# Optimization experiments

Measured on AMD Instinct MI355X. Metric: run time of the kernel, lower is better.

The kernel has to match this reference:

```python
import jax, jax.numpy as jnp
import numpy as np

GAM1 = 1.0
GAM2 = 1.0
EPS = 0.01


def setup_inputs() -> dict:
    key = jax.random.key(0)
    k1, k2 = jax.random.split(key)
    m, p, k = 262144, 128, 10
    x = jax.random.normal(k1, (m, p), dtype=jnp.float32)
    y = jax.random.randint(k2, (m,), 0, k, dtype=jnp.int32)
    return {"x": x, "y": y, "num_classes": k}


def reference(x, y, num_classes):
    m, p = x.shape
    I = jnp.eye(p, dtype=x.dtype)
    scalar = p / (m * EPS)

    # W = x.T, so W @ W.T == x.T @ x  (p x p Gram)
    cov = x.T @ x
    discrimn_empi = jnp.linalg.slogdet(I + GAM1 * scalar * cov)[1] / 2.0
    discrimn_theo = jnp.linalg.slogdet(I + scalar * cov)[1] / 2.0

    # per-class compress loss: logdet(I + p/(n_j*eps) * W_j W_j^T) * n_j / m
    onehot = jax.nn.one_hot(y, num_classes, dtype=x.dtype)  # [m, k]
    counts = onehot.sum(axis=0)                             # [k]

    def class_cov(col):  # col: [m] 0/1 mask for one class
        return (x * col[:, None]).T @ x  # [p, p]

    covs = jax.lax.map(class_cov, onehot.T)  # [k, p, p], sequential over k classes

    safe_counts = jnp.maximum(counts, 1.0)
    scal = p / (safe_counts * EPS)                              # [k]
    lds = jnp.linalg.slogdet(I[None] + scal[:, None, None] * covs)[1]  # [k]
    compress = jnp.sum(jnp.where(counts > 0, lds * counts / m, 0.0)) / 2.0

    total_loss_empi = GAM2 * (-discrimn_empi) + compress
    return total_loss_empi, discrimn_empi, discrimn_theo, compress
```

## Files before the change

### kernel.cpp

```cpp
#include <hip/hip_runtime.h>

#define K 10
#define P 128
#define EPSV 0.01f
#define GAM1 1.0f
#define GAM2 1.0f
#define CH 256
#define SK 32
#define KS 36
#define NSTG (CH / SK)
#define SORTCH 2048
#define NTHR 256

typedef __attribute__((ext_vector_type(8))) short bf16x8;
typedef __attribute__((ext_vector_type(4))) short s16x4;
typedef __attribute__((ext_vector_type(4))) float f32x4;

static __device__ __forceinline__ short f2bf(float f) {
    unsigned u = __float_as_uint(f);
    u = (u + 0x7FFFu + ((u >> 16) & 1u)) >> 16;
    return (short)u;
}

static __device__ __forceinline__ float rdlane(float v, int srclane) {
    return __int_as_float(__builtin_amdgcn_readlane(__float_as_int(v), srclane));
}

__global__ void hist_kernel(const int* __restrict__ y, int* __restrict__ blk_counts, int m) {
    __shared__ int h[K];
    int t = threadIdx.x;
    if (t < K) h[t] = 0;
    __syncthreads();
    int base = blockIdx.x * SORTCH;
    int rows = min(SORTCH, m - base);
    for (int i = t; i < rows; i += NTHR) atomicAdd(&h[y[base + i]], 1);
    __syncthreads();
    if (t < K) blk_counts[blockIdx.x * K + t] = h[t];
}

__global__ void scan_kernel(const int* __restrict__ blk_counts, int* __restrict__ blk_offsets,
                            int* __restrict__ counts, int* __restrict__ pstart, int nb) {
    __shared__ int s[K][128];
    __shared__ int sps[K + 1];
    int t = threadIdx.x;
    int own[K];
    if (t < 128) {
        for (int c = 0; c < K; ++c) {
            int v = (t < nb) ? blk_counts[t * K + c] : 0;
            own[c] = v;
            s[c][t] = v;
        }
    }
    __syncthreads();
    for (int off = 1; off < 128; off <<= 1) {
        int tmp[K];
        if (t < 128)
            for (int c = 0; c < K; ++c) tmp[c] = (t >= off) ? s[c][t - off] : 0;
        __syncthreads();
        if (t < 128)
            for (int c = 0; c < K; ++c) s[c][t] += tmp[c];
        __syncthreads();
    }
    if (t == 0) {
        int run = 0;
        for (int c = 0; c < K; ++c) {
            sps[c] = run;
            int tot = s[c][127];
            counts[c] = tot;
            pstart[c] = run;
            run += ((tot + CH - 1) / CH) * CH;
        }
        sps[K] = run;
        pstart[K] = run;
    }
    __syncthreads();
    if (t < nb)
        for (int c = 0; c < K; ++c)
            blk_offsets[t * K + c] = sps[c] + s[c][t] - own[c];
}

__global__ void scatter_kernel(const int* __restrict__ y, const int* __restrict__ blk_offsets,
                               int* __restrict__ perm, int m) {
    __shared__ int cur[K];
    int t = threadIdx.x;
    if (t < K) cur[t] = blk_offsets[blockIdx.x * K + t];
    __syncthreads();
    int base = blockIdx.x * SORTCH;
    int rows = min(SORTCH, m - base);
    for (int i = t; i < rows; i += NTHR) {
        int row = base + i;
        int pos = atomicAdd(&cur[y[row]], 1);
        perm[pos] = row;
    }
}

__global__ __launch_bounds__(NTHR, 4) void gram_kernel(const float* __restrict__ x,
                                                       const int* __restrict__ perm,
                                                       const int* __restrict__ pstart,
                                                       const int* __restrict__ counts,
                                                       float* __restrict__ grams) {
    __shared__ int pm[CH];
    __shared__ short xsT[2][P * KS];
    int t = threadIdx.x;
    int base = blockIdx.x * CH;
    int cls = 0;
#pragma unroll
    for (int c = 1; c < K; ++c)
        if (base >= pstart[c]) cls = c;
    const int limit = pstart[cls] + counts[cls];
    pm[t] = perm[base + t];

    const int lane = t & 63;
    const int wave = t >> 6;
    const int m16 = lane & 15;
    const int quad = lane >> 4;
    const int wr = wave >> 1;
    const int wc = wave & 1;
    const int c2 = lane;

    f32x4 acc[4][4];
#pragma unroll
    for (int a = 0; a < 4; ++a)
#pragma unroll
        for (int b = 0; b < 4; ++b) acc[a][b] = (f32x4){0.f, 0.f, 0.f, 0.f};

    __syncthreads();

    float2 v[8];
#pragma unroll
    for (int ii = 0; ii < 8; ++ii) {
        int pos = wave * 8 + ii;
        float2 val; val.x = 0.f; val.y = 0.f;
        if (base + pos < limit) {
            int r = pm[pos];
            val = ((const float2*)(x + (size_t)r * P))[c2];
        }
        v[ii] = val;
    }

#pragma unroll 2
    for (int s = 0; s < NSTG; ++s) {
        short* xb = &xsT[s & 1][0];
        short b0[8], b1[8];
#pragma unroll
        for (int ii = 0; ii < 8; ++ii) { b0[ii] = f2bf(v[ii].x); b1[ii] = f2bf(v[ii].y); }
        {
            int col0 = 2 * c2, col1 = 2 * c2 + 1;
            int kb = wave * 8;
#pragma unroll
            for (int q = 0; q < 2; ++q) {
                s16x4 w0 = {b0[q * 4], b0[q * 4 + 1], b0[q * 4 + 2], b0[q * 4 + 3]};
                s16x4 w1 = {b1[q * 4], b1[q * 4 + 1], b1[q * 4 + 2], b1[q * 4 + 3]};
                *(s16x4*)&xb[col0 * KS + kb + q * 4] = w0;
                *(s16x4*)&xb[col1 * KS + kb + q * 4] = w1;
            }
        }
        __syncthreads();
        if (s + 1 < NSTG) {
            int sb = (s + 1) * SK;
#pragma unroll
            for (int ii = 0; ii < 8; ++ii) {
                int pos = sb + wave * 8 + ii;
                float2 val; val.x = 0.f; val.y = 0.f;
                if (base + pos < limit) {
                    int r = pm[pos];
                    val = ((const float2*)(x + (size_t)r * P))[c2];
                }
                v[ii] = val;
            }
        }
        int k0 = quad * 8;
        bf16x8 bfr[4];
#pragma unroll
        for (int b = 0; b < 4; ++b) {
            int colB = wc * 64 + b * 16 + m16;
            union { bf16x8 v8; s16x4 h[2]; } u;
            u.h[0] = *(const s16x4*)&xb[colB * KS + k0];
            u.h[1] = *(const s16x4*)&xb[colB * KS + k0 + 4];
            bfr[b] = u.v8;
        }
#pragma unroll
        for (int a = 0; a < 4; ++a) {
            int colA = wr * 64 + a * 16 + m16;
            union { bf16x8 v8; s16x4 h[2]; } u;
            u.h[0] = *(const s16x4*)&xb[colA * KS + k0];
            u.h[1] = *(const s16x4*)&xb[colA * KS + k0 + 4];
            bf16x8 af = u.v8;
#pragma unroll
            for (int b = 0; b < 4; ++b)
                acc[a][b] = __builtin_amdgcn_mfma_f32_16x16x32_bf16(af, bfr[b], acc[a][b], 0, 0, 0);
        }
    }
    float* g = grams + (size_t)cls * P * P;
#pragma unroll
    for (int a = 0; a < 4; ++a)
#pragma unroll
        for (int b = 0; b < 4; ++b)
#pragma unroll
            for (int r = 0; r < 4; ++r) {
                int gi = wr * 64 + a * 16 + quad * 4 + r;
                int gj = wc * 64 + b * 16 + m16;
                if (gi <= gj) atomicAdd(&g[gi * P + gj], acc[a][b][r]);
            }
}

__global__ void sum_kernel(const float* __restrict__ grams, float* __restrict__ gsum) {
    int idx = blockIdx.x * 256 + threadIdx.x;
    float s = 0.f;
#pragma unroll
    for (int c = 0; c < K; ++c) s += grams[c * P * P + idx];
    gsum[idx] = s;
}

__global__ __launch_bounds__(256, 1) void logdet_kernel(const float* __restrict__ grams,
                                                        const float* __restrict__ gsum,
                                                        const int* __restrict__ counts,
                                                        float* __restrict__ logd, int m) {
    __shared__ float A[P * P];
    int t = threadIdx.x, b = blockIdx.x;
    float scale;
    if (b == 0) scale = GAM1 * (float)P / ((float)m * EPSV);
    else if (b == 1) scale = (float)P / ((float)m * EPSV);
    else {
        float cnt = (float)counts[b - 2];
        if (cnt < 1.f) cnt = 1.f;
        scale = (float)P / (cnt * EPSV);
    }
    const float* src = (b < 2) ? gsum : (grams + (size_t)(b - 2) * P * P);
    for (int idx = t; idx < P * P; idx += 256) {
        int i = idx >> 7, c = idx & (P - 1);
        int s2 = (i <= c) ? idx : (c * P + i);
        A[idx] = scale * src[s2] + ((i == c) ? 1.f : 0.f);
    }
    __syncthreads();

    const int lane = t & 63;
    const int wid = t >> 6;
    float lsum = 0.f;

    for (int bs = 0; bs < 4; ++bs) {
        const int j0 = bs * 32;
        if (wid == 0) {
            float a[32];
            if (lane < 32) {
#pragma unroll
                for (int cc = 0; cc < 8; ++cc)
                    *(f32x4*)&a[cc * 4] = *(f32x4*)&A[(j0 + lane) * P + j0 + cc * 4];
            } else {
#pragma unroll
                for (int cc = 0; cc < 32; ++cc) a[cc] = 0.f;
            }
            float myinv = 0.f;
#pragma unroll
            for (int tt = 0; tt < 32; ++tt) {
                float utt = rdlane(a[tt], tt);
                float inv = __builtin_amdgcn_rcpf(utt);
                lsum += __logf(utt);
                if (lane == tt) myinv = inv;
                bool act = (lane < 32) && (lane > tt);
                float lm = act ? a[tt] * inv : 0.f;
                if (act) a[tt] = lm;
#pragma unroll
                for (int k2 = tt + 1; k2 < 32; ++k2) {
                    float utk = rdlane(a[k2], tt);
                    a[k2] -= lm * utk;
                }
            }
            if (lane < 32) A[(j0 + lane) * P + j0 + lane] = myinv;

            if (bs < 3) {
                int nc = P - j0 - 32;
                int c0 = j0 + 32 + lane;
                int c1 = c0 + 64;
                bool v0 = lane < nc;
                bool v1 = lane + 64 < nc;
                int c0a = v0 ? c0 : (j0 + 32);
                int c1a = v1 ? c1 : (j0 + 32);
                float ua[32], ub[32];
#pragma unroll
                for (int j = 0; j < 32; ++j) {
                    ua[j] = A[(j0 + j) * P + c0a];
                    ub[j] = A[(j0 + j) * P + c1a];
                }
#pragma unroll
                for (int j = 0; j < 32; ++j) {
#pragma unroll
                    for (int t2 = 0; t2 < j; ++t2) {
                        float ljt = rdlane(a[t2], j);
                        ua[j] -= ljt * ua[t2];
                        ub[j] -= ljt * ub[t2];
                    }
                }
#pragma unroll
                for (int j = 0; j < 32; ++j) {
                    if (v0) A[(j0 + j) * P + c0] = ua[j];
                    if (v1) A[(j0 + j) * P + c1] = ub[j];
                }
            }
        }
        __syncthreads();

        if (bs < 3) {
            int nc = P - j0 - 32;
            int nt = nc >> 2;
            int ntiles = nt * nt;
            for (int tile = t; tile < ntiles; tile += 256) {
                int ti = tile / nt, tk = tile - ti * nt;
                int i0 = j0 + 32 + ti * 4, k0 = j0 + 32 + tk * 4;
                f32x4 acc0 = {0, 0, 0, 0}, acc1 = {0, 0, 0, 0};
                f32x4 acc2 = {0, 0, 0, 0}, acc3 = {0, 0, 0, 0};
#pragma unroll
                for (int j = 0; j < 32; ++j) {
                    const float* row = &A[(j0 + j) * P];
                    float invd = row[j0 + j];
                    f32x4 ui = *(const f32x4*)&row[i0];
                    f32x4 uk = *(const f32x4*)&row[k0];
                    uk *= invd;
                    acc0 += ui[0] * uk;
                    acc1 += ui[1] * uk;
                    acc2 += ui[2] * uk;
                    acc3 += ui[3] * uk;
                }
                f32x4* r0 = (f32x4*)&A[(i0 + 0) * P + k0];
                f32x4* r1 = (f32x4*)&A[(i0 + 1) * P + k0];
                f32x4* r2 = (f32x4*)&A[(i0 + 2) * P + k0];
                f32x4* r3 = (f32x4*)&A[(i0 + 3) * P + k0];
                *r0 -= acc0; *r1 -= acc1; *r2 -= acc2; *r3 -= acc3;
            }
            __syncthreads();
        }
    }
    if (t == 0) logd[b] = lsum;
}

__global__ void final_kernel(const float* __restrict__ logd, const int* __restrict__ counts,
                             float* __restrict__ out, int m) {
    if (threadIdx.x == 0 && blockIdx.x == 0) {
        float empi = 0.5f * logd[0];
        float theo = 0.5f * logd[1];
        float comp = 0.f;
        for (int c = 0; c < K; ++c) {
            float cnt = (float)counts[c];
            if (cnt > 0.f) comp += logd[2 + c] * cnt / (float)m;
        }
        comp *= 0.5f;
        out[0] = GAM2 * (-empi) + comp;
        out[1] = empi;
        out[2] = theo;
        out[3] = comp;
    }
}

extern "C" void kernel_launch(void* const* d_in, const int* in_sizes, int n_in,
                              void* d_out, int out_size, void* d_ws, size_t ws_size,
                              hipStream_t stream) {
    const float* x = (const float*)d_in[0];
    const int* y = (const int*)d_in[1];
    int m = in_sizes[1];
    int nbs = (m + SORTCH - 1) / SORTCH;
    int nbg = (m + CH - 1) / CH + K;

    char* ws = (char*)d_ws;
    float* grams = (float*)ws;
    float* gsum = (float*)(ws + 655360);
    float* logd = (float*)(ws + 720896);
    int* counts = (int*)(ws + 720960);
    int* pstart = (int*)(ws + 721024);
    int* blk_counts = (int*)(ws + 721152);
    int* blk_offsets = (int*)(ws + 721152 + (size_t)nbs * K * 4);
    int* perm = (int*)(ws + 721152 + 2 * (size_t)nbs * K * 4);

    hipMemsetAsync(ws, 0, 655360, stream);

    hist_kernel<<<nbs, NTHR, 0, stream>>>(y, blk_counts, m);
    scan_kernel<<<1, NTHR, 0, stream>>>(blk_counts, blk_offsets, counts, pstart, nbs);
    scatter_kernel<<<nbs, NTHR, 0, stream>>>(y, blk_offsets, perm, m);
    gram_kernel<<<nbg, NTHR, 0, stream>>>(x, perm, pstart, counts, grams);
    sum_kernel<<<P * P / 256, 256, 0, stream>>>(grams, gsum);
    logdet_kernel<<<K + 2, 256, 0, stream>>>(grams, gsum, counts, logd, m);
    final_kernel<<<1, 1, 0, stream>>>(logd, counts, (float*)d_out, m);
}
```

Before: 314.2 us.

## Replace gram atomics with per-block partials and separate reduce kernel

Each gram block now writes its full 128x128 partial Gram tile to a workspace slot instead of atomically adding the upper triangle into per-class accumulators. A new reduce kernel then sums each class's block partials into the class Gram. The memset of the accumulators is dropped because the reduce overwrites them. Blocks also grow to 512 threads with a 512-row chunk and 64-row k-stages (two MFMA k-steps per stage), so each wave now covers a 32x64 output tile. This removes atomic contention on the shared class Grams, at the cost of extra global traffic for the partial tiles and one more kernel launch. The reduce assumes class start offsets in the sorted order are aligned to the chunk size.

```diff
diff --git a/kernel.cpp b/kernel.cpp
--- a/kernel.cpp
+++ b/kernel.cpp
@@ -5,12 +5,13 @@
 #define EPSV 0.01f
 #define GAM1 1.0f
 #define GAM2 1.0f
-#define CH 256
-#define SK 32
-#define KS 36
+#define CH 512
+#define SK 64
+#define KS 68
 #define NSTG (CH / SK)
 #define SORTCH 2048
 #define NTHR 256
+#define GTHR 512
 
 typedef __attribute__((ext_vector_type(8))) short bf16x8;
 typedef __attribute__((ext_vector_type(4))) short s16x4;
@@ -94,11 +95,11 @@
     }
 }
 
-__global__ __launch_bounds__(NTHR, 4) void gram_kernel(const float* __restrict__ x,
+__global__ __launch_bounds__(GTHR, 4) void gram_kernel(const float* __restrict__ x,
                                                        const int* __restrict__ perm,
                                                        const int* __restrict__ pstart,
                                                        const int* __restrict__ counts,
-                                                       float* __restrict__ grams) {
+                                                       float* __restrict__ partial) {
     __shared__ int pm[CH];
     __shared__ short xsT[2][P * KS];
     int t = threadIdx.x;
@@ -118,9 +119,9 @@
     const int wc = wave & 1;
     const int c2 = lane;
 
-    f32x4 acc[4][4];
-#pragma unroll
-    for (int a = 0; a < 4; ++a)
+    f32x4 acc[2][4];
+#pragma unroll
+    for (int a = 0; a < 2; ++a)
 #pragma unroll
         for (int b = 0; b < 4; ++b) acc[a][b] = (f32x4){0.f, 0.f, 0.f, 0.f};
 
@@ -138,14 +139,13 @@
         v[ii] = val;
     }
 
-#pragma unroll 2
     for (int s = 0; s < NSTG; ++s) {
         short* xb = &xsT[s & 1][0];
         short b0[8], b1[8];
 #pragma unroll
         for (int ii = 0; ii < 8; ++ii) { b0[ii] = f2bf(v[ii].x); b1[ii] = f2bf(v[ii].y); }
         {
-            int col0 = 2 * c2, col1 = 2 * c2 + 1;
+            int col0 = 2 * c2, col1 = col0 + 1;
             int kb = wave * 8;
 #pragma unroll
             for (int q = 0; q < 2; ++q) {
@@ -169,39 +169,53 @@
                 v[ii] = val;
             }
         }
-        int k0 = quad * 8;
-        bf16x8 bfr[4];
-#pragma unroll
-        for (int b = 0; b < 4; ++b) {
-            int colB = wc * 64 + b * 16 + m16;
-            union { bf16x8 v8; s16x4 h[2]; } u;
-            u.h[0] = *(const s16x4*)&xb[colB * KS + k0];
-            u.h[1] = *(const s16x4*)&xb[colB * KS + k0 + 4];
-            bfr[b] = u.v8;
-        }
-#pragma unroll
-        for (int a = 0; a < 4; ++a) {
-            int colA = wr * 64 + a * 16 + m16;
-            union { bf16x8 v8; s16x4 h[2]; } u;
-            u.h[0] = *(const s16x4*)&xb[colA * KS + k0];
-            u.h[1] = *(const s16x4*)&xb[colA * KS + k0 + 4];
-            bf16x8 af = u.v8;
-#pragma unroll
-            for (int b = 0; b < 4; ++b)
-                acc[a][b] = __builtin_amdgcn_mfma_f32_16x16x32_bf16(af, bfr[b], acc[a][b], 0, 0, 0);
-        }
-    }
-    float* g = grams + (size_t)cls * P * P;
-#pragma unroll
-    for (int a = 0; a < 4; ++a)
+#pragma unroll
+        for (int kk = 0; kk < 2; ++kk) {
+            int k0 = kk * 32 + quad * 8;
+            bf16x8 bfr[4];
+#pragma unroll
+            for (int b = 0; b < 4; ++b) {
+                int colB = wc * 64 + b * 16 + m16;
+                union { bf16x8 v8; s16x4 h[2]; } u;
+                u.h[0] = *(const s16x4*)&xb[colB * KS + k0];
+                u.h[1] = *(const s16x4*)&xb[colB * KS + k0 + 4];
+                bfr[b] = u.v8;
+            }
+#pragma unroll
+            for (int a = 0; a < 2; ++a) {
+                int colA = wr * 32 + a * 16 + m16;
+                union { bf16x8 v8; s16x4 h[2]; } u;
+                u.h[0] = *(const s16x4*)&xb[colA * KS + k0];
+                u.h[1] = *(const s16x4*)&xb[colA * KS + k0 + 4];
+                bf16x8 af = u.v8;
+#pragma unroll
+                for (int b = 0; b < 4; ++b)
+                    acc[a][b] = __builtin_amdgcn_mfma_f32_16x16x32_bf16(af, bfr[b], acc[a][b], 0, 0, 0);
+            }
+        }
+    }
+    float* pt = partial + (size_t)blockIdx.x * (P * P);
+#pragma unroll
+    for (int a = 0; a < 2; ++a)
 #pragma unroll
         for (int b = 0; b < 4; ++b)
 #pragma unroll
             for (int r = 0; r < 4; ++r) {
-                int gi = wr * 64 + a * 16 + quad * 4 + r;
+                int gi = wr * 32 + a * 16 + quad * 4 + r;
                 int gj = wc * 64 + b * 16 + m16;
-                if (gi <= gj) atomicAdd(&g[gi * P + gj], acc[a][b][r]);
-            }
+                pt[gi * P + gj] = acc[a][b][r];
+            }
+}
+
+__global__ void reduce_kernel(const float* __restrict__ partial, const int* __restrict__ pstart,
+                              float* __restrict__ grams) {
+    int c = blockIdx.x >> 6;
+    int e = ((blockIdx.x & 63) << 8) + threadIdx.x;
+    int b0 = pstart[c] / CH;
+    int b1 = pstart[c + 1] / CH;
+    float s = 0.f;
+    for (int b = b0; b < b1; ++b) s += partial[(size_t)b * (P * P) + e];
+    grams[(size_t)c * (P * P) + e] = s;
 }
 
 __global__ void sum_kernel(const float* __restrict__ grams, float* __restrict__ gsum) {
@@ -369,13 +383,14 @@
     int* blk_counts = (int*)(ws + 721152);
     int* blk_offsets = (int*)(ws + 721152 + (size_t)nbs * K * 4);
     int* perm = (int*)(ws + 721152 + 2 * (size_t)nbs * K * 4);
-
-    hipMemsetAsync(ws, 0, 655360, stream);
+    float* partial = (float*)(ws + (2u << 20));
+
 
     hist_kernel<<<nbs, NTHR, 0, stream>>>(y, blk_counts, m);
     scan_kernel<<<1, NTHR, 0, stream>>>(blk_counts, blk_offsets, counts, pstart, nbs);
     scatter_kernel<<<nbs, NTHR, 0, stream>>>(y, blk_offsets, perm, m);
-    gram_kernel<<<nbg, NTHR, 0, stream>>>(x, perm, pstart, counts, grams);
+    gram_kernel<<<nbg, GTHR, 0, stream>>>(x, perm, pstart, counts, partial);
+    reduce_kernel<<<K * (P * P / 256), 256, 0, stream>>>(partial, pstart, grams);
     sum_kernel<<<P * P / 256, 256, 0, stream>>>(grams, gsum);
     logdet_kernel<<<K + 2, 256, 0, stream>>>(grams, gsum, counts, logd, m);
     final_kernel<<<1, 1, 0, stream>>>(logd, counts, (float*)d_out, m);
```

Result: faster. 303.2 us (-3.5%).
